# Performance work log

Measured on AMD Instinct MI355X. Metric: run time of the kernel, lower is better.

The kernel has to match this reference:

```python
import jax, jax.numpy as jnp
import numpy as np

HEAD_NUM = 16

def setup_inputs() -> dict:
    key = jax.random.key(0)
    ks = jax.random.split(key, 5)
    B, N, D = 2, 2048, 1024
    x = jax.random.normal(ks[0], (B, N, D), dtype=jnp.float32)
    scale = 0.02
    W_q = jax.random.normal(ks[1], (D, D), dtype=jnp.float32) * scale
    W_k = jax.random.normal(ks[2], (D, D), dtype=jnp.float32) * scale
    W_v = jax.random.normal(ks[3], (D, D), dtype=jnp.float32) * scale
    W_o = jax.random.normal(ks[4], (D, D), dtype=jnp.float32) * scale
    return {"x": x, "W_q": W_q, "W_k": W_k, "W_v": W_v, "W_o": W_o}

def reference(x, W_q, W_k, W_v, W_o):
    B, N, D = x.shape
    H = HEAD_NUM
    hd = D // H  # head_dim
    inv_sqrt_hd = 1.0 / np.sqrt(hd).astype(np.float32)

    def split_head(t):
        # einops 'b n (d h) -> b h n d' : head index is the INNER factor
        return t.reshape(B, N, hd, H).transpose(0, 3, 1, 2)  # [B,H,N,hd]

    # nn.Linear(bias=False): y = x @ W.T
    Q = split_head(x @ W_q.T)
    K = split_head(x @ W_k.T)
    V = split_head(x @ W_v.T)

    scores = jnp.einsum('bhnd,bhmd->bhnm', Q, K) * inv_sqrt_hd  # [B,H,N,N]
    attn = jax.nn.softmax(scores, axis=-1)
    heads = jnp.einsum('bhnm,bhmd->bhnd', attn, V)  # [B,H,N,hd]

    # einops 'b h n d -> b n (h d)' : head index is the OUTER factor here
    concat = heads.transpose(0, 2, 1, 3).reshape(B, N, D)
    return concat @ W_o.T
```

## Files before the change

### kernel.cpp

```cpp
#include <hip/hip_runtime.h>
#include <hip/hip_bf16.h>

typedef __bf16 bf16_t;
typedef __attribute__((ext_vector_type(8))) __bf16 bf16x8;
typedef __attribute__((ext_vector_type(4))) __bf16 bf16x4;
typedef __attribute__((ext_vector_type(4))) float f32x4;
typedef __attribute__((ext_vector_type(16))) float f32x16;

#define MFMA16(A,B,C) __builtin_amdgcn_mfma_f32_16x16x32_bf16((A),(B),(C),0,0,0)
#define MFMA32(A,B,C) __builtin_amdgcn_mfma_f32_32x32x16_bf16((A),(B),(C),0,0,0)

#define BATCH 2
#define SEQ 2048
#define DMODEL 1024
#define NHEAD 16
#define HDIM 64
#define MROWS (BATCH * SEQ)

__device__ __forceinline__ void async16(const bf16_t* g, bf16_t* l) {
    __builtin_amdgcn_global_load_lds(
        (const __attribute__((address_space(1))) unsigned int*)g,
        (__attribute__((address_space(3))) unsigned int*)l, 16, 0, 0);
}

__device__ __forceinline__ bf16x8 ldsA32(const bf16_t* base, int row, int chunk) {
    return *(const bf16x8*)&base[row * 32 + ((chunk ^ ((row >> 1) & 3)) << 3)];
}
__device__ __forceinline__ bf16x8 ldsA64(const bf16_t* base, int row, int chunk) {
    return *(const bf16x8*)&base[row * 64 + ((chunk ^ (row & 7)) << 3)];
}

__device__ __forceinline__ unsigned pk(float a, float b) {
    union { unsigned u; bf16_t h[2]; } t;
    t.h[0] = (bf16_t)a;
    t.h[1] = (bf16_t)b;
    return t.u;
}

__global__ void split_kernel(const float* __restrict__ x, const float* __restrict__ Wq,
                             const float* __restrict__ Wk, const float* __restrict__ Wv,
                             const float* __restrict__ Wo, bf16_t* __restrict__ xh,
                             bf16_t* __restrict__ wh) {
    int blk = blockIdx.x;
    if (blk < 4096) {
        int i = blk * 256 + threadIdx.x;
        f32x4 v = ((const f32x4*)x)[i];
        bf16x4 h;
#pragma unroll
        for (int c = 0; c < 4; ++c) h[c] = (bf16_t)v[c];
        ((bf16x4*)xh)[i] = h;
        return;
    }
    int e = blk - 4096;
    int z = e >> 10;
    int i = (e & 1023) * 256 + threadIdx.x;
    const float* src = (z == 0) ? Wq : (z == 1) ? Wk : (z == 2) ? Wv : Wo;
    const float scale = (z == 0) ? 0.125f * 1.44269504088896f : 1.0f;
    int row = i >> 8, col4 = i & 255;
    int r_src;
    if (z < 3) {
        int h = row >> 6, d = row & 63;
        r_src = 16 * d + h;
    } else {
        r_src = row;
    }
    f32x4 v = ((const f32x4*)src)[r_src * 256 + col4];
    bf16x4 h4;
#pragma unroll
    for (int c = 0; c < 4; ++c) h4[c] = (bf16_t)(v[c] * scale);
    ((bf16x4*)(wh + (size_t)z * DMODEL * DMODEL))[i] = h4;
}

__global__ __launch_bounds__(256)
void gemm_qkv_kernel(const bf16_t* __restrict__ Ah, const bf16_t* __restrict__ Bh0,
                     bf16_t* __restrict__ Coh0, int M, int Nn, int Kk) {
    __shared__ __align__(16) bf16_t smem[2][8192];

    const int z = blockIdx.z;
    const bf16_t* Bh = Bh0 + (size_t)z * Nn * Kk;
    const int m0 = blockIdx.y * 128, n0 = blockIdx.x * 128;
    const int tid = threadIdx.x;
    const int wave = tid >> 6, lane = tid & 63, lq = lane >> 4, ln = lane & 15;
    const int wr = wave >> 1, wc = wave & 1;

    const bf16_t* g_ptr[4];
    int l_off[4];
#pragma unroll
    for (int q = 0; q < 4; ++q) {
        int e = wave * 4 + q;
        int a = e >> 3, u = e & 7;
        int C = u * 64 + lane;
        int r = C >> 2, p = C & 3;
        int c = p ^ ((r >> 1) & 3);
        g_ptr[q] = (a == 0 ? Ah + (size_t)(m0 + r) * Kk
                           : Bh + (size_t)(n0 + r) * Kk) + c * 8;
        l_off[q] = a * 4096 + u * 512;
    }

    f32x4 acc[4][4] = {};

#pragma unroll
    for (int q = 0; q < 4; ++q)
        async16(g_ptr[q], &smem[0][l_off[q]]);

    const int NIT = Kk / 32;
    for (int j = 0; j < NIT; ++j) {
        __syncthreads();
        if (j + 1 < NIT) {
#pragma unroll
            for (int q = 0; q < 4; ++q)
                async16(g_ptr[q] + (j + 1) * 32, &smem[(j + 1) & 1][l_off[q]]);
        }
        const bf16_t* cur = smem[j & 1];

        bf16x8 ah[4], bh[4];
#pragma unroll
        for (int t = 0; t < 4; ++t) {
            ah[t] = ldsA32(cur, wr * 64 + t * 16 + ln, lq);
            bh[t] = ldsA32(cur + 4096, wc * 64 + t * 16 + ln, lq);
        }
#pragma unroll
        for (int tm = 0; tm < 4; ++tm)
#pragma unroll
            for (int tn = 0; tn < 4; ++tn)
                acc[tm][tn] = MFMA16(ah[tm], bh[tn], acc[tm][tn]);
    }

#pragma unroll
    for (int tm = 0; tm < 4; ++tm)
#pragma unroll
        for (int tn = 0; tn < 4; ++tn)
#pragma unroll
            for (int p = 0; p < 4; ++p) {
                int gm = m0 + wr * 64 + tm * 16 + lq * 4 + p;
                int gn = n0 + wc * 64 + tn * 16 + ln;
                Coh0[(size_t)z * M * Nn + (size_t)gm * Nn + gn] =
                    (bf16_t)acc[tm][tn][p];
            }
}

__global__ __launch_bounds__(256)
void gemm_out_kernel(const bf16_t* __restrict__ Ah, const bf16_t* __restrict__ Bh,
                     float* __restrict__ Cf, int M, int Nn, int Kk) {
    __shared__ __align__(16) bf16_t smem[2][6144];

    const int m0 = blockIdx.y * 64, n0 = blockIdx.x * 128;
    const int tid = threadIdx.x;
    const int wave = tid >> 6, lane = tid & 63, lq = lane >> 4, ln = lane & 15;
    const int wr = wave >> 1, wc = wave & 1;

    const bf16_t* g_ptr[3];
    int l_off[3];
#pragma unroll
    for (int q = 0; q < 3; ++q) {
        int e = wave * 3 + q;
        const bf16_t* arr;
        int u, rowbase, lb;
        if (e < 4) { arr = Ah; u = e;     rowbase = m0; lb = 0; }
        else       { arr = Bh; u = e - 4; rowbase = n0; lb = 2048; }
        int r = u * 16 + (lane >> 2), p = lane & 3;
        int c = p ^ ((r >> 1) & 3);
        g_ptr[q] = arr + (size_t)(rowbase + r) * Kk + c * 8;
        l_off[q] = lb + u * 512;
    }

    f32x4 acc[2][4] = {};

#pragma unroll
    for (int q = 0; q < 3; ++q)
        async16(g_ptr[q], &smem[0][l_off[q]]);

    const int NIT = Kk / 32;
    for (int j = 0; j < NIT; ++j) {
        __syncthreads();
        if (j + 1 < NIT) {
#pragma unroll
            for (int q = 0; q < 3; ++q)
                async16(g_ptr[q] + (j + 1) * 32, &smem[(j + 1) & 1][l_off[q]]);
        }
        const bf16_t* cur = smem[j & 1];

        bf16x8 ah[2], bh[4];
#pragma unroll
        for (int t = 0; t < 2; ++t)
            ah[t] = ldsA32(cur, wr * 32 + t * 16 + ln, lq);
#pragma unroll
        for (int t = 0; t < 4; ++t)
            bh[t] = ldsA32(cur + 2048, wc * 64 + t * 16 + ln, lq);
#pragma unroll
        for (int tm = 0; tm < 2; ++tm)
#pragma unroll
            for (int tn = 0; tn < 4; ++tn)
                acc[tm][tn] = MFMA16(ah[tm], bh[tn], acc[tm][tn]);
    }

#pragma unroll
    for (int tm = 0; tm < 2; ++tm)
#pragma unroll
        for (int tn = 0; tn < 4; ++tn)
#pragma unroll
            for (int p = 0; p < 4; ++p) {
                int gm = m0 + wr * 32 + tm * 16 + lq * 4 + p;
                int gn = n0 + wc * 64 + tn * 16 + ln;
                Cf[(size_t)gm * Nn + gn] = acc[tm][tn][p];
            }
}

__global__ __launch_bounds__(256)
void vtrans_kernel(const bf16_t* __restrict__ Vn, bf16_t* __restrict__ Vt) {
    __shared__ bf16_t t[64][66];
    const int bh = blockIdx.y;
    const int b = bh >> 4, h = bh & 15;
    const int n0 = blockIdx.x * 64;
    const int tid = threadIdx.x;
#pragma unroll
    for (int it = 0; it < 2; ++it) {
        int c = it * 256 + tid;
        int r = c >> 3, p = c & 7;
        *(bf16x8*)&t[r][p * 8] =
            *(const bf16x8*)&Vn[((size_t)(b * SEQ + n0 + r)) * DMODEL + h * HDIM + p * 8];
    }
    __syncthreads();
#pragma unroll
    for (int it = 0; it < 2; ++it) {
        int c = it * 256 + tid;
        int d = c >> 3, p = c & 7;
        bf16x8 v;
#pragma unroll
        for (int e = 0; e < 8; ++e) v[e] = t[p * 8 + e][d];
        *(bf16x8*)&Vt[((size_t)(bh * HDIM + d)) * SEQ + n0 + p * 8] = v;
    }
}

__global__ __launch_bounds__(512, 4)
void attn_kernel(const bf16_t* __restrict__ Qh, const bf16_t* __restrict__ Kh,
                 const bf16_t* __restrict__ Vt, bf16_t* __restrict__ Ch) {
    __shared__ __align__(16) bf16_t smem[2][2][8192];

    const int bh = blockIdx.y;
    const int b = bh >> 4, h = bh & 15;
    const int q0 = blockIdx.x * 128;
    const int tid = threadIdx.x;
    const int g = tid >> 8;
    const int wv = (tid >> 6) & 3;
    const int lane = tid & 63;
    const int ln32 = lane & 31, hl = lane >> 5;

    bf16x8 qfh[4];
    {
        size_t qrow = ((size_t)(b * SEQ + q0 + wv * 32 + ln32)) * DMODEL +
                      h * HDIM + hl * 8;
#pragma unroll
        for (int c = 0; c < 4; ++c)
            qfh[c] = *(const bf16x8*)&Qh[qrow + c * 16];
    }
    bf16x8 ones;
#pragma unroll
    for (int e = 0; e < 8; ++e) ones[e] = (bf16_t)1.0f;

    bf16_t* gsm = &smem[g][0][0];
    const bf16_t* g_base[4];
    int l_off[4];
    size_t g_step[4];
#pragma unroll
    for (int q = 0; q < 4; ++q) {
        int e = wv * 4 + q;
        int a = e >> 3, u = e & 7;
        int r = u * 8 + (lane >> 3), p = lane & 7;
        int c = p ^ (r & 7);
        if (a == 0) {
            g_base[q] = Kh + ((size_t)(b * SEQ + g * 1024 + r)) * DMODEL +
                        h * HDIM + c * 8;
            l_off[q] = u * 512;
            g_step[q] = (size_t)64 * DMODEL;
        } else {
            g_base[q] = Vt + ((size_t)(bh * HDIM + r)) * SEQ + g * 1024 + c * 8;
            l_off[q] = 4096 + u * 512;
            g_step[q] = 64;
        }
    }

    f32x16 o[2], o_ones;
#pragma unroll
    for (int dt = 0; dt < 2; ++dt)
#pragma unroll
        for (int r = 0; r < 16; ++r) o[dt][r] = 0.0f;
#pragma unroll
    for (int r = 0; r < 16; ++r) o_ones[r] = 0.0f;

#pragma unroll
    for (int q = 0; q < 4; ++q)
        async16(g_base[q], gsm + l_off[q]);

    for (int j = 0; j < 16; ++j) {
        __syncthreads();
        if (j < 15) {
#pragma unroll
            for (int q = 0; q < 4; ++q)
                async16(g_base[q] + (j + 1) * g_step[q],
                        gsm + ((j + 1) & 1) * 8192 + l_off[q]);
        }
        const bf16_t* Kc = gsm + (j & 1) * 8192;
        const bf16_t* Vc = Kc + 4096;

        bf16x8 pfrag[4];
#pragma unroll
        for (int kt = 0; kt < 2; ++kt) {
            f32x16 st;
#pragma unroll
            for (int r = 0; r < 16; ++r) st[r] = 0.0f;
#pragma unroll
            for (int c = 0; c < 4; ++c) {
                bf16x8 kh = ldsA64(Kc, kt * 32 + ln32, 2 * c + hl);
                st = MFMA32(kh, qfh[c], st);
            }
            float pexp[16];
#pragma unroll
            for (int r = 0; r < 16; ++r)
                pexp[r] = __builtin_amdgcn_exp2f(st[r]);
#pragma unroll
            for (int s1 = 0; s1 < 2; ++s1) {
                unsigned lo01 = pk(pexp[8 * s1 + 0], pexp[8 * s1 + 1]);
                unsigned lo23 = pk(pexp[8 * s1 + 2], pexp[8 * s1 + 3]);
                unsigned hi01 = pk(pexp[8 * s1 + 4], pexp[8 * s1 + 5]);
                unsigned hi23 = pk(pexp[8 * s1 + 6], pexp[8 * s1 + 7]);
                unsigned sa = hl ? lo01 : hi01;
                unsigned sb = hl ? lo23 : hi23;
                unsigned ra = (unsigned)__shfl_xor((int)sa, 32);
                unsigned rb = (unsigned)__shfl_xor((int)sb, 32);
                union { bf16x8 v; unsigned u[4]; } outv;
                outv.u[0] = hl ? ra : lo01;
                outv.u[1] = hl ? rb : lo23;
                outv.u[2] = hl ? hi01 : ra;
                outv.u[3] = hl ? hi23 : rb;
                pfrag[kt * 2 + s1] = outv.v;
            }
        }
#pragma unroll
        for (int s = 0; s < 4; ++s) {
            bf16x8 va0 = ldsA64(Vc, ln32, 2 * s + hl);
            bf16x8 va1 = ldsA64(Vc, 32 + ln32, 2 * s + hl);
            o[0] = MFMA32(va0, pfrag[s], o[0]);
            o[1] = MFMA32(va1, pfrag[s], o[1]);
            o_ones = MFMA32(ones, pfrag[s], o_ones);
        }
    }

    float rs = o_ones[0];

    __syncthreads();
    float* cbuf = (float*)smem;
    float* rbuf = cbuf + 8192;
    if (g == 1) {
#pragma unroll
        for (int dt = 0; dt < 2; ++dt)
#pragma unroll
            for (int r = 0; r < 16; ++r) {
                int d = dt * 32 + (r & 3) + 8 * (r >> 2) + 4 * hl;
                cbuf[d * 128 + wv * 32 + ln32] = o[dt][r];
            }
        if (hl == 0) rbuf[wv * 32 + ln32] = rs;
    }
    __syncthreads();
    float inv = 0.0f;
    if (g == 0) {
#pragma unroll
        for (int dt = 0; dt < 2; ++dt)
#pragma unroll
            for (int r = 0; r < 16; ++r) {
                int d = dt * 32 + (r & 3) + 8 * (r >> 2) + 4 * hl;
                o[dt][r] += cbuf[d * 128 + wv * 32 + ln32];
            }
        inv = 1.0f / (rs + rbuf[wv * 32 + ln32]);
    }
    __syncthreads();
    float* fbuf = (float*)smem;
    if (g == 0) {
#pragma unroll
        for (int dh = 0; dh < 2; ++dh)
#pragma unroll
            for (int r = 0; r < 16; ++r) {
                int d_loc = (r & 3) + 8 * (r >> 2) + 4 * hl;
                fbuf[dh * 4224 + wv * 1056 + ln32 * 33 + d_loc] = o[dh][r] * inv;
            }
    }
    __syncthreads();
    {
        int gw = tid >> 6;
        int dh = gw >> 2, w = gw & 3;
#pragma unroll
        for (int qq = 0; qq < 16; ++qq) {
            int qrow = hl * 16 + qq;
            float v = fbuf[dh * 4224 + w * 1056 + qrow * 33 + ln32];
            size_t gidx = ((size_t)(b * SEQ + q0 + w * 32 + qrow)) * DMODEL +
                          h * HDIM + dh * 32 + ln32;
            Ch[gidx] = (bf16_t)v;
        }
    }
}

extern "C" void kernel_launch(void* const* d_in, const int* in_sizes, int n_in,
                              void* d_out, int out_size, void* d_ws, size_t ws_size,
                              hipStream_t stream) {
    const float* x  = (const float*)d_in[0];
    const float* Wq = (const float*)d_in[1];
    const float* Wk = (const float*)d_in[2];
    const float* Wv = (const float*)d_in[3];
    const float* Wo = (const float*)d_in[4];
    float* out = (float*)d_out;

    char* ws = (char*)d_ws;
    size_t off = 0;
    auto alloc = [&](size_t bytes) -> bf16_t* {
        bf16_t* p = (bf16_t*)(ws + off);
        off += (bytes + 255) & ~(size_t)255;
        return p;
    };
    const size_t XE = (size_t)MROWS * DMODEL;
    const size_t WE = (size_t)DMODEL * DMODEL;

    bf16_t* xh  = alloc(XE * 2);
    bf16_t* wh  = alloc(4 * WE * 2);
    bf16_t* qnh = alloc(3 * XE * 2);
    bf16_t* vth = alloc(XE * 2);
    bf16_t* ch  = alloc(XE * 2);
    (void)ws_size; (void)in_sizes; (void)n_in; (void)out_size;

    split_kernel<<<8192, 256, 0, stream>>>(x, Wq, Wk, Wv, Wo, xh, wh);

    gemm_qkv_kernel<<<dim3(DMODEL / 128, MROWS / 128, 3), 256, 0, stream>>>(
        xh, wh, qnh, MROWS, DMODEL, DMODEL);

    vtrans_kernel<<<dim3(SEQ / 64, BATCH * NHEAD), 256, 0, stream>>>(qnh + 2 * XE, vth);

    attn_kernel<<<dim3(SEQ / 128, BATCH * NHEAD), 512, 0, stream>>>(
        qnh, qnh + XE, vth, ch);

    gemm_out_kernel<<<dim3(DMODEL / 128, MROWS / 64), 256, 0, stream>>>(
        ch, wh + 3 * WE, out, MROWS, DMODEL, DMODEL);
}
```

Baseline: 184.7 us.

## Fuse V transpose into QKV GEMM, remap blocks per XCD, drop ones-MFMA rowsum

The QKV GEMM now writes V directly in transposed per-head layout, so the separate transpose kernel and its round trip through global memory go away. All three main kernels switch to 1D grids whose block index is remapped so that neighbouring tiles land on the same XCD, aiming for better L2 reuse of shared operands. The attention kernel replaces the extra MFMA against a ones vector with a scalar accumulation of the exponentials plus a cross-half shuffle. It also precomputes the swizzled LDS offsets and advances global pointers incrementally. The transposed V store is an uncoalesced 4-element strided write, which could cost some GEMM store bandwidth.

```diff
diff --git a/kernel.cpp b/kernel.cpp
--- a/kernel.cpp
+++ b/kernel.cpp
@@ -25,9 +25,6 @@
 
 __device__ __forceinline__ bf16x8 ldsA32(const bf16_t* base, int row, int chunk) {
     return *(const bf16x8*)&base[row * 32 + ((chunk ^ ((row >> 1) & 3)) << 3)];
-}
-__device__ __forceinline__ bf16x8 ldsA64(const bf16_t* base, int row, int chunk) {
-    return *(const bf16x8*)&base[row * 64 + ((chunk ^ (row & 7)) << 3)];
 }
 
 __device__ __forceinline__ unsigned pk(float a, float b) {
@@ -73,12 +70,21 @@
 
 __global__ __launch_bounds__(256)
 void gemm_qkv_kernel(const bf16_t* __restrict__ Ah, const bf16_t* __restrict__ Bh0,
-                     bf16_t* __restrict__ Coh0, int M, int Nn, int Kk) {
+                     bf16_t* __restrict__ Coh0, bf16_t* __restrict__ Vt,
+                     int M, int Nn, int Kk) {
     __shared__ __align__(16) bf16_t smem[2][8192];
 
-    const int z = blockIdx.z;
+    const int id = blockIdx.x;
+    const int xcd = id & 7;
+    const int t = id >> 3;
+    const int n0i = t & 7;
+    const int u = t >> 3;
+    const int z = u >> 2;
+    const int m0g = u & 3;
+    const int m0 = (m0g * 8 + xcd) * 128;
+    const int n0 = n0i * 128;
+
     const bf16_t* Bh = Bh0 + (size_t)z * Nn * Kk;
-    const int m0 = blockIdx.y * 128, n0 = blockIdx.x * 128;
     const int tid = threadIdx.x;
     const int wave = tid >> 6, lane = tid & 63, lq = lane >> 4, ln = lane & 15;
     const int wr = wave >> 1, wc = wave & 1;
@@ -88,13 +94,13 @@
 #pragma unroll
     for (int q = 0; q < 4; ++q) {
         int e = wave * 4 + q;
-        int a = e >> 3, u = e & 7;
-        int C = u * 64 + lane;
+        int a = e >> 3, uu = e & 7;
+        int C = uu * 64 + lane;
         int r = C >> 2, p = C & 3;
         int c = p ^ ((r >> 1) & 3);
         g_ptr[q] = (a == 0 ? Ah + (size_t)(m0 + r) * Kk
                            : Bh + (size_t)(n0 + r) * Kk) + c * 8;
-        l_off[q] = a * 4096 + u * 512;
+        l_off[q] = a * 4096 + uu * 512;
     }
 
     f32x4 acc[4][4] = {};
@@ -115,9 +121,9 @@
 
         bf16x8 ah[4], bh[4];
 #pragma unroll
-        for (int t = 0; t < 4; ++t) {
-            ah[t] = ldsA32(cur, wr * 64 + t * 16 + ln, lq);
-            bh[t] = ldsA32(cur + 4096, wc * 64 + t * 16 + ln, lq);
+        for (int tt = 0; tt < 4; ++tt) {
+            ah[tt] = ldsA32(cur, wr * 64 + tt * 16 + ln, lq);
+            bh[tt] = ldsA32(cur + 4096, wc * 64 + tt * 16 + ln, lq);
         }
 #pragma unroll
         for (int tm = 0; tm < 4; ++tm)
@@ -126,17 +132,33 @@
                 acc[tm][tn] = MFMA16(ah[tm], bh[tn], acc[tm][tn]);
     }
 
-#pragma unroll
-    for (int tm = 0; tm < 4; ++tm)
-#pragma unroll
-        for (int tn = 0; tn < 4; ++tn)
-#pragma unroll
-            for (int p = 0; p < 4; ++p) {
-                int gm = m0 + wr * 64 + tm * 16 + lq * 4 + p;
+    if (z != 2) {
+#pragma unroll
+        for (int tm = 0; tm < 4; ++tm)
+#pragma unroll
+            for (int tn = 0; tn < 4; ++tn)
+#pragma unroll
+                for (int p = 0; p < 4; ++p) {
+                    int gm = m0 + wr * 64 + tm * 16 + lq * 4 + p;
+                    int gn = n0 + wc * 64 + tn * 16 + ln;
+                    Coh0[(size_t)z * M * Nn + (size_t)gm * Nn + gn] =
+                        (bf16_t)acc[tm][tn][p];
+                }
+    } else {
+#pragma unroll
+        for (int tm = 0; tm < 4; ++tm)
+#pragma unroll
+            for (int tn = 0; tn < 4; ++tn) {
                 int gn = n0 + wc * 64 + tn * 16 + ln;
-                Coh0[(size_t)z * M * Nn + (size_t)gm * Nn + gn] =
-                    (bf16_t)acc[tm][tn][p];
-            }
+                int hh = gn >> 6, dd = gn & 63;
+                int gm0 = m0 + wr * 64 + tm * 16 + lq * 4;
+                int bb = gm0 >> 11, nn = gm0 & 2047;
+                bf16x4 v4;
+#pragma unroll
+                for (int p = 0; p < 4; ++p) v4[p] = (bf16_t)acc[tm][tn][p];
+                *(bf16x4*)&Vt[(((size_t)(bb * NHEAD + hh)) * HDIM + dd) * SEQ + nn] = v4;
+            }
+    }
 }
 
 __global__ __launch_bounds__(256)
@@ -144,7 +166,14 @@
                      float* __restrict__ Cf, int M, int Nn, int Kk) {
     __shared__ __align__(16) bf16_t smem[2][6144];
 
-    const int m0 = blockIdx.y * 64, n0 = blockIdx.x * 128;
+    const int id = blockIdx.x;
+    const int xcd = id & 7;
+    const int t = id >> 3;
+    const int n0i = t & 7;
+    const int m0g = t >> 3;
+    const int m0 = (m0g * 8 + xcd) * 64;
+    const int n0 = n0i * 128;
+
     const int tid = threadIdx.x;
     const int wave = tid >> 6, lane = tid & 63, lq = lane >> 4, ln = lane & 15;
     const int wr = wave >> 1, wc = wave & 1;
@@ -182,11 +211,11 @@
 
         bf16x8 ah[2], bh[4];
 #pragma unroll
-        for (int t = 0; t < 2; ++t)
-            ah[t] = ldsA32(cur, wr * 32 + t * 16 + ln, lq);
-#pragma unroll
-        for (int t = 0; t < 4; ++t)
-            bh[t] = ldsA32(cur + 2048, wc * 64 + t * 16 + ln, lq);
+        for (int tt = 0; tt < 2; ++tt)
+            ah[tt] = ldsA32(cur, wr * 32 + tt * 16 + ln, lq);
+#pragma unroll
+        for (int tt = 0; tt < 4; ++tt)
+            bh[tt] = ldsA32(cur + 2048, wc * 64 + tt * 16 + ln, lq);
 #pragma unroll
         for (int tm = 0; tm < 2; ++tm)
 #pragma unroll
@@ -206,40 +235,16 @@
             }
 }
 
-__global__ __launch_bounds__(256)
-void vtrans_kernel(const bf16_t* __restrict__ Vn, bf16_t* __restrict__ Vt) {
-    __shared__ bf16_t t[64][66];
-    const int bh = blockIdx.y;
-    const int b = bh >> 4, h = bh & 15;
-    const int n0 = blockIdx.x * 64;
-    const int tid = threadIdx.x;
-#pragma unroll
-    for (int it = 0; it < 2; ++it) {
-        int c = it * 256 + tid;
-        int r = c >> 3, p = c & 7;
-        *(bf16x8*)&t[r][p * 8] =
-            *(const bf16x8*)&Vn[((size_t)(b * SEQ + n0 + r)) * DMODEL + h * HDIM + p * 8];
-    }
-    __syncthreads();
-#pragma unroll
-    for (int it = 0; it < 2; ++it) {
-        int c = it * 256 + tid;
-        int d = c >> 3, p = c & 7;
-        bf16x8 v;
-#pragma unroll
-        for (int e = 0; e < 8; ++e) v[e] = t[p * 8 + e][d];
-        *(bf16x8*)&Vt[((size_t)(bh * HDIM + d)) * SEQ + n0 + p * 8] = v;
-    }
-}
-
 __global__ __launch_bounds__(512, 4)
 void attn_kernel(const bf16_t* __restrict__ Qh, const bf16_t* __restrict__ Kh,
                  const bf16_t* __restrict__ Vt, bf16_t* __restrict__ Ch) {
     __shared__ __align__(16) bf16_t smem[2][2][8192];
 
-    const int bh = blockIdx.y;
+    const int id = blockIdx.x;
+    const int bh = ((id >> 7) << 3) | (id & 7);
+    const int qt = (id >> 3) & 15;
     const int b = bh >> 4, h = bh & 15;
-    const int q0 = blockIdx.x * 128;
+    const int q0 = qt * 128;
     const int tid = threadIdx.x;
     const int g = tid >> 8;
     const int wv = (tid >> 6) & 3;
@@ -254,12 +259,15 @@
         for (int c = 0; c < 4; ++c)
             qfh[c] = *(const bf16x8*)&Qh[qrow + c * 16];
     }
-    bf16x8 ones;
-#pragma unroll
-    for (int e = 0; e < 8; ++e) ones[e] = (bf16_t)1.0f;
+
+    const int xrow = ln32 * 64;
+    int xc[4];
+#pragma unroll
+    for (int c = 0; c < 4; ++c)
+        xc[c] = (((2 * c + hl) ^ (ln32 & 7)) << 3) + xrow;
 
     bf16_t* gsm = &smem[g][0][0];
-    const bf16_t* g_base[4];
+    const bf16_t* g_cur[4];
     int l_off[4];
     size_t g_step[4];
 #pragma unroll
@@ -269,36 +277,38 @@
         int r = u * 8 + (lane >> 3), p = lane & 7;
         int c = p ^ (r & 7);
         if (a == 0) {
-            g_base[q] = Kh + ((size_t)(b * SEQ + g * 1024 + r)) * DMODEL +
-                        h * HDIM + c * 8;
+            g_cur[q] = Kh + ((size_t)(b * SEQ + g * 1024 + r)) * DMODEL +
+                       h * HDIM + c * 8;
             l_off[q] = u * 512;
             g_step[q] = (size_t)64 * DMODEL;
         } else {
-            g_base[q] = Vt + ((size_t)(bh * HDIM + r)) * SEQ + g * 1024 + c * 8;
+            g_cur[q] = Vt + ((size_t)(bh * HDIM + r)) * SEQ + g * 1024 + c * 8;
             l_off[q] = 4096 + u * 512;
             g_step[q] = 64;
         }
     }
 
-    f32x16 o[2], o_ones;
+    f32x16 o[2];
 #pragma unroll
     for (int dt = 0; dt < 2; ++dt)
 #pragma unroll
         for (int r = 0; r < 16; ++r) o[dt][r] = 0.0f;
-#pragma unroll
-    for (int r = 0; r < 16; ++r) o_ones[r] = 0.0f;
-
-#pragma unroll
-    for (int q = 0; q < 4; ++q)
-        async16(g_base[q], gsm + l_off[q]);
+    float rs = 0.0f;
+
+#pragma unroll
+    for (int q = 0; q < 4; ++q) {
+        async16(g_cur[q], gsm + l_off[q]);
+        g_cur[q] += g_step[q];
+    }
 
     for (int j = 0; j < 16; ++j) {
         __syncthreads();
         if (j < 15) {
 #pragma unroll
-            for (int q = 0; q < 4; ++q)
-                async16(g_base[q] + (j + 1) * g_step[q],
-                        gsm + ((j + 1) & 1) * 8192 + l_off[q]);
+            for (int q = 0; q < 4; ++q) {
+                async16(g_cur[q], gsm + ((j + 1) & 1) * 8192 + l_off[q]);
+                g_cur[q] += g_step[q];
+            }
         }
         const bf16_t* Kc = gsm + (j & 1) * 8192;
         const bf16_t* Vc = Kc + 4096;
@@ -311,13 +321,15 @@
             for (int r = 0; r < 16; ++r) st[r] = 0.0f;
 #pragma unroll
             for (int c = 0; c < 4; ++c) {
-                bf16x8 kh = ldsA64(Kc, kt * 32 + ln32, 2 * c + hl);
+                bf16x8 kh = *(const bf16x8*)&Kc[kt * 2048 + xc[c]];
                 st = MFMA32(kh, qfh[c], st);
             }
             float pexp[16];
 #pragma unroll
-            for (int r = 0; r < 16; ++r)
+            for (int r = 0; r < 16; ++r) {
                 pexp[r] = __builtin_amdgcn_exp2f(st[r]);
+                rs += pexp[r];
+            }
 #pragma unroll
             for (int s1 = 0; s1 < 2; ++s1) {
                 unsigned lo01 = pk(pexp[8 * s1 + 0], pexp[8 * s1 + 1]);
@@ -338,15 +350,14 @@
         }
 #pragma unroll
         for (int s = 0; s < 4; ++s) {
-            bf16x8 va0 = ldsA64(Vc, ln32, 2 * s + hl);
-            bf16x8 va1 = ldsA64(Vc, 32 + ln32, 2 * s + hl);
+            bf16x8 va0 = *(const bf16x8*)&Vc[xc[s]];
+            bf16x8 va1 = *(const bf16x8*)&Vc[2048 + xc[s]];
             o[0] = MFMA32(va0, pfrag[s], o[0]);
             o[1] = MFMA32(va1, pfrag[s], o[1]);
-            o_ones = MFMA32(ones, pfrag[s], o_ones);
-        }
-    }
-
-    float rs = o_ones[0];
+        }
+    }
+
+    rs += __shfl_xor(rs, 32);
 
     __syncthreads();
     float* cbuf = (float*)smem;
@@ -428,14 +439,9 @@
 
     split_kernel<<<8192, 256, 0, stream>>>(x, Wq, Wk, Wv, Wo, xh, wh);
 
-    gemm_qkv_kernel<<<dim3(DMODEL / 128, MROWS / 128, 3), 256, 0, stream>>>(
-        xh, wh, qnh, MROWS, DMODEL, DMODEL);
-
-    vtrans_kernel<<<dim3(SEQ / 64, BATCH * NHEAD), 256, 0, stream>>>(qnh + 2 * XE, vth);
-
-    attn_kernel<<<dim3(SEQ / 128, BATCH * NHEAD), 512, 0, stream>>>(
-        qnh, qnh + XE, vth, ch);
-
-    gemm_out_kernel<<<dim3(DMODEL / 128, MROWS / 64), 256, 0, stream>>>(
-        ch, wh + 3 * WE, out, MROWS, DMODEL, DMODEL);
-}
+    gemm_qkv_kernel<<<768, 256, 0, stream>>>(xh, wh, qnh, vth, MROWS, DMODEL, DMODEL);
+
+    attn_kernel<<<512, 512, 0, stream>>>(qnh, qnh + XE, vth, ch);
+
+    gemm_out_kernel<<<512, 256, 0, stream>>>(ch, wh + 3 * WE, out, MROWS, DMODEL, DMODEL);
+}
```

Measured after the change: 179.4 us, median of 2. 2.9% less time.
